# Kernel tuning notes

Measured on AMD Instinct MI355X. Metric: run time of the kernel, lower is better.

Reference implementation:

```python
import jax, jax.numpy as jnp
import numpy as np

TEMPERATURE = 8.0  # sqrt(d_head=64)


def setup_inputs() -> dict:
    key = jax.random.key(0)
    ks = jax.random.split(key, 6)
    shape = (4, 16, 2048, 64)  # [B, H, L, d_head]
    names = ["q_real", "q_imag", "k_real", "k_imag", "v_real", "v_imag"]
    return {n: jax.random.normal(k, shape, dtype=jnp.float32) for n, k in zip(names, ks)}


def reference(q_real, q_imag, k_real, k_imag, v_real, v_imag):
    # attn = | (q / T) @ conj(k)^H |
    # complex matmul with b = conj(k)^T: br = k_r^T, bi = -k_i^T
    qr = q_real / TEMPERATURE
    qi = q_imag / TEMPERATURE
    # [B,H,Lq,Lk]
    s_real = jnp.einsum("bhqd,bhkd->bhqk", qr, k_real) + jnp.einsum("bhqd,bhkd->bhqk", qi, k_imag)
    s_imag = jnp.einsum("bhqd,bhkd->bhqk", qi, k_real) - jnp.einsum("bhqd,bhkd->bhqk", qr, k_imag)
    attn = jax.nn.softmax(jnp.sqrt(s_real * s_real + s_imag * s_imag), axis=-1)
    # dropout p=0.0 (eval) -> identity
    out_real = jnp.einsum("bhqk,bhkd->bhqd", attn, v_real)
    out_imag = jnp.einsum("bhqk,bhkd->bhqd", attn, v_imag)
    # torch.view_as_complex(stack([real, imag], -1)) -> represent as stacked last dim
    output = jnp.stack([out_real, out_imag], axis=-1)  # [B,H,L,d,2]
    return output, attn
```

## Files before the change

kernel.cpp:

```cpp
#include <hip/hip_runtime.h>
#include <hip/hip_bf16.h>

constexpr int kL  = 2048;
constexpr int kD  = 64;
constexpr int kBH = 64;
constexpr size_t kAttnOff = (size_t)kBH * kL * kD * 2;

typedef __bf16 bf16x8 __attribute__((ext_vector_type(8)));
typedef __bf16 bf16x4 __attribute__((ext_vector_type(4)));
typedef float  f32x4  __attribute__((ext_vector_type(4)));
typedef unsigned int u32x4 __attribute__((ext_vector_type(4)));

static __device__ inline bf16x8 neg8(bf16x8 v) {
  u32x4 t = __builtin_bit_cast(u32x4, v);
  t ^= 0x80008000u;
  return __builtin_bit_cast(bf16x8, t);
}

__global__ __launch_bounds__(256) void transpose_v_kernel(
    const float* __restrict__ vr_g, const float* __restrict__ vi_g,
    __hip_bfloat16* __restrict__ vt_r, __hip_bfloat16* __restrict__ vt_i)
{
  __shared__ __align__(16) char lds_raw[2 * 8192];
  char* tr = lds_raw;
  char* ti = lds_raw + 8192;

  const int tid = threadIdx.x;
  const int bh  = blockIdx.x >> 5;
  const int kb  = blockIdx.x & 31;
  const int k0  = kb * 64;

  {
    const int krow = tid >> 2;
    const int d0   = (tid & 3) << 4;
    const size_t gb = ((size_t)bh * kL + k0 + krow) * kD + d0;
    const int base = krow * 128;
    const int swz  = (krow & 7) << 4;
    {
      float4 x0 = *(const float4*)(vr_g + gb);
      float4 x1 = *(const float4*)(vr_g + gb + 4);
      float4 x2 = *(const float4*)(vr_g + gb + 8);
      float4 x3 = *(const float4*)(vr_g + gb + 12);
      bf16x8 p0, p1;
      p0[0]=(__bf16)x0.x; p0[1]=(__bf16)x0.y; p0[2]=(__bf16)x0.z; p0[3]=(__bf16)x0.w;
      p0[4]=(__bf16)x1.x; p0[5]=(__bf16)x1.y; p0[6]=(__bf16)x1.z; p0[7]=(__bf16)x1.w;
      p1[0]=(__bf16)x2.x; p1[1]=(__bf16)x2.y; p1[2]=(__bf16)x2.z; p1[3]=(__bf16)x2.w;
      p1[4]=(__bf16)x3.x; p1[5]=(__bf16)x3.y; p1[6]=(__bf16)x3.z; p1[7]=(__bf16)x3.w;
      *(bf16x8*)(tr + base + ((d0 * 2) ^ swz))      = p0;
      *(bf16x8*)(tr + base + ((d0 * 2 + 16) ^ swz)) = p1;
    }
    {
      float4 x0 = *(const float4*)(vi_g + gb);
      float4 x1 = *(const float4*)(vi_g + gb + 4);
      float4 x2 = *(const float4*)(vi_g + gb + 8);
      float4 x3 = *(const float4*)(vi_g + gb + 12);
      bf16x8 p0, p1;
      p0[0]=(__bf16)x0.x; p0[1]=(__bf16)x0.y; p0[2]=(__bf16)x0.z; p0[3]=(__bf16)x0.w;
      p0[4]=(__bf16)x1.x; p0[5]=(__bf16)x1.y; p0[6]=(__bf16)x1.z; p0[7]=(__bf16)x1.w;
      p1[0]=(__bf16)x2.x; p1[1]=(__bf16)x2.y; p1[2]=(__bf16)x2.z; p1[3]=(__bf16)x2.w;
      p1[4]=(__bf16)x3.x; p1[5]=(__bf16)x3.y; p1[6]=(__bf16)x3.z; p1[7]=(__bf16)x3.w;
      *(bf16x8*)(ti + base + ((d0 * 2) ^ swz))      = p0;
      *(bf16x8*)(ti + base + ((d0 * 2 + 16) ^ swz)) = p1;
    }
  }
  __syncthreads();

  {
    const int d  = tid >> 2;
    const int kc = (tid & 3) << 4;
    const size_t tb = ((size_t)bh * 32 + kb) * 8192;
    char* outr = (char*)vt_r + tb + d * 128;
    char* outi = (char*)vt_i + tb + d * 128;
    const int oswz = (d & 7) << 4;
    bf16x8 pr0, pr1, pi0, pi1;
#pragma unroll
    for (int j = 0; j < 8; ++j) {
      const int k1 = kc + j;
      const int k2 = kc + 8 + j;
      const int b1 = k1 * 128 + ((d * 2) ^ ((k1 & 7) << 4));
      const int b2 = k2 * 128 + ((d * 2) ^ ((k2 & 7) << 4));
      pr0[j] = *(const __bf16*)(tr + b1);
      pr1[j] = *(const __bf16*)(tr + b2);
      pi0[j] = *(const __bf16*)(ti + b1);
      pi1[j] = *(const __bf16*)(ti + b2);
    }
    *(bf16x8*)(outr + ((kc * 2) ^ oswz))        = pr0;
    *(bf16x8*)(outr + ((kc * 2 + 16) ^ oswz))   = pr1;
    *(bf16x8*)(outi + ((kc * 2) ^ oswz))        = pi0;
    *(bf16x8*)(outi + ((kc * 2 + 16) ^ oswz))   = pi1;
  }
}

template<int WS>
__global__ __launch_bounds__(256) void qk_exp_kernel(
    const float* __restrict__ qr_g, const float* __restrict__ qi_g,
    const float* __restrict__ kr_g, const float* __restrict__ ki_g,
    __hip_bfloat16* __restrict__ ews, float* __restrict__ attn,
    float* __restrict__ rowsum)
{
  __shared__ __align__(16) char lds_raw[16384 + 4 * 4096];
  char* kr_l = lds_raw;
  char* ki_l = lds_raw + 8192;
  char* e_l  = lds_raw + 16384 + (threadIdx.x >> 6) * 4096;

  const int tid  = threadIdx.x;
  const int wave = tid >> 6;
  const int lane = tid & 63;
  const int g    = lane >> 4;
  const int r    = lane & 15;

  const int bid = blockIdx.x;
  const int nid = (bid & 7) * 128 + (bid >> 3);
  const int bh  = nid >> 4;
  const int q0w = (nid & 15) * 128 + wave * 32;

  bf16x8 aqr[2][2], aqi[2][2];
#pragma unroll
  for (int qt = 0; qt < 2; ++qt) {
    const size_t qbase = ((size_t)bh * kL + q0w + qt * 16 + r) * kD + g * 8;
#pragma unroll
    for (int f = 0; f < 2; ++f) {
      float4 x0 = *(const float4*)(qr_g + qbase + f * 32);
      float4 x1 = *(const float4*)(qr_g + qbase + f * 32 + 4);
      float4 y0 = *(const float4*)(qi_g + qbase + f * 32);
      float4 y1 = *(const float4*)(qi_g + qbase + f * 32 + 4);
      float xr[8] = {x0.x, x0.y, x0.z, x0.w, x1.x, x1.y, x1.z, x1.w};
      float xi[8] = {y0.x, y0.y, y0.z, y0.w, y1.x, y1.y, y1.z, y1.w};
#pragma unroll
      for (int i = 0; i < 8; ++i) {
        aqr[qt][f][i] = (__bf16)(xr[i] * 0.125f);
        aqi[qt][f][i] = (__bf16)(xi[i] * 0.125f);
      }
    }
  }

  float rs[2] = {0.f, 0.f};

  for (int k0 = 0; k0 < kL; k0 += 64) {
    __syncthreads();
    {
      const int row = tid >> 2;
      const int d0  = (tid & 3) << 4;
      const size_t gb = ((size_t)bh * kL + k0 + row) * kD + d0;
      const int base = row * 128;
      const int swz  = (row & 7) << 4;
      {
        float4 x0 = *(const float4*)(kr_g + gb);
        float4 x1 = *(const float4*)(kr_g + gb + 4);
        float4 x2 = *(const float4*)(kr_g + gb + 8);
        float4 x3 = *(const float4*)(kr_g + gb + 12);
        bf16x8 p0, p1;
        p0[0]=(__bf16)x0.x; p0[1]=(__bf16)x0.y; p0[2]=(__bf16)x0.z; p0[3]=(__bf16)x0.w;
        p0[4]=(__bf16)x1.x; p0[5]=(__bf16)x1.y; p0[6]=(__bf16)x1.z; p0[7]=(__bf16)x1.w;
        p1[0]=(__bf16)x2.x; p1[1]=(__bf16)x2.y; p1[2]=(__bf16)x2.z; p1[3]=(__bf16)x2.w;
        p1[4]=(__bf16)x3.x; p1[5]=(__bf16)x3.y; p1[6]=(__bf16)x3.z; p1[7]=(__bf16)x3.w;
        *(bf16x8*)(kr_l + base + ((d0 * 2) ^ swz))      = p0;
        *(bf16x8*)(kr_l + base + ((d0 * 2 + 16) ^ swz)) = p1;
      }
      {
        float4 x0 = *(const float4*)(ki_g + gb);
        float4 x1 = *(const float4*)(ki_g + gb + 4);
        float4 x2 = *(const float4*)(ki_g + gb + 8);
        float4 x3 = *(const float4*)(ki_g + gb + 12);
        bf16x8 p0, p1;
        p0[0]=(__bf16)x0.x; p0[1]=(__bf16)x0.y; p0[2]=(__bf16)x0.z; p0[3]=(__bf16)x0.w;
        p0[4]=(__bf16)x1.x; p0[5]=(__bf16)x1.y; p0[6]=(__bf16)x1.z; p0[7]=(__bf16)x1.w;
        p1[0]=(__bf16)x2.x; p1[1]=(__bf16)x2.y; p1[2]=(__bf16)x2.z; p1[3]=(__bf16)x2.w;
        p1[4]=(__bf16)x3.x; p1[5]=(__bf16)x3.y; p1[6]=(__bf16)x3.z; p1[7]=(__bf16)x3.w;
        *(bf16x8*)(ki_l + base + ((d0 * 2) ^ swz))      = p0;
        *(bf16x8*)(ki_l + base + ((d0 * 2 + 16) ^ swz)) = p1;
      }
    }
    __syncthreads();

#pragma unroll
    for (int s = 0; s < 4; ++s) {
      const int krow = s * 16 + r;
      const int swz  = (krow & 7) << 4;
      bf16x8 bkr[2], bki[2], bkin[2];
#pragma unroll
      for (int f = 0; f < 2; ++f) {
        const int byte = krow * 128 + (((f * 32 + g * 8) * 2) ^ swz);
        bkr[f]  = *(const bf16x8*)(kr_l + byte);
        bki[f]  = *(const bf16x8*)(ki_l + byte);
        bkin[f] = neg8(bki[f]);
      }
#pragma unroll
      for (int qt = 0; qt < 2; ++qt) {
        f32x4 accr = {0.f, 0.f, 0.f, 0.f};
        f32x4 acci = {0.f, 0.f, 0.f, 0.f};
#pragma unroll
        for (int f = 0; f < 2; ++f) {
          accr = __builtin_amdgcn_mfma_f32_16x16x32_bf16(bkr[f],  aqr[qt][f], accr, 0, 0, 0);
          accr = __builtin_amdgcn_mfma_f32_16x16x32_bf16(bki[f],  aqi[qt][f], accr, 0, 0, 0);
          acci = __builtin_amdgcn_mfma_f32_16x16x32_bf16(bkr[f],  aqi[qt][f], acci, 0, 0, 0);
          acci = __builtin_amdgcn_mfma_f32_16x16x32_bf16(bkin[f], aqr[qt][f], acci, 0, 0, 0);
        }
        float e[4];
#pragma unroll
        for (int i = 0; i < 4; ++i)
          e[i] = __expf(sqrtf(accr[i] * accr[i] + acci[i] * acci[i]));
        rs[qt] += (e[0] + e[1]) + (e[2] + e[3]);
        bf16x4 pe;
#pragma unroll
        for (int i = 0; i < 4; ++i) pe[i] = (__bf16)e[i];
        const int row = qt * 16 + r;
        *(bf16x4*)(e_l + row * 128 + (((s * 16 + g * 4) * 2) ^ ((row & 7) << 4))) = pe;
      }
    }

#pragma unroll
    for (int m = 0; m < 4; ++m) {
      const int row  = m * 8 + (lane >> 3);
      const int byte = row * 128 + (((lane & 7) * 16) ^ ((row & 7) << 4));
      bf16x8 v = *(const bf16x8*)(e_l + byte);
      const size_t base = ((size_t)bh * kL + q0w + row) * kL + k0 + (lane & 7) * 8;
      if (WS) {
        *(bf16x8*)((__bf16*)ews + base) = v;
      } else {
        float4 w0, w1;
        w0.x=(float)v[0]; w0.y=(float)v[1]; w0.z=(float)v[2]; w0.w=(float)v[3];
        w1.x=(float)v[4]; w1.y=(float)v[5]; w1.z=(float)v[6]; w1.w=(float)v[7];
        *(float4*)(attn + base)     = w0;
        *(float4*)(attn + base + 4) = w1;
      }
    }
  }

#pragma unroll
  for (int qt = 0; qt < 2; ++qt) {
    rs[qt] += __shfl_xor(rs[qt], 16, 64);
    rs[qt] += __shfl_xor(rs[qt], 32, 64);
  }
  if (lane < 16) {
#pragma unroll
    for (int qt = 0; qt < 2; ++qt)
      rowsum[(size_t)bh * kL + q0w + qt * 16 + lane] = rs[qt];
  }
}

template<int WS, int VT>
__global__ __launch_bounds__(256) void pv_kernel(
    const float* __restrict__ vr_g, const float* __restrict__ vi_g,
    const __hip_bfloat16* __restrict__ vt_r, const __hip_bfloat16* __restrict__ vt_i,
    const __hip_bfloat16* __restrict__ ews, float* __restrict__ attn,
    const float* __restrict__ rowsum, float* __restrict__ out)
{
  __shared__ __align__(16) char lds_raw[2 * 8192];
  char* vr_l = lds_raw;
  char* vi_l = lds_raw + 8192;

  const int tid  = threadIdx.x;
  const int wave = tid >> 6;
  const int lane = tid & 63;
  const int g    = lane >> 4;
  const int r    = lane & 15;

  const int bid = blockIdx.x;
  const int nid = (bid & 7) * 128 + (bid >> 3);
  const int bh  = nid >> 4;
  const int q0w = (nid & 15) * 128 + wave * 32;

  float invA[2];
#pragma unroll
  for (int qt = 0; qt < 2; ++qt)
    invA[qt] = 1.0f / rowsum[(size_t)bh * kL + q0w + qt * 16 + r];

  f32x4 o_r[2][4], o_i[2][4];
#pragma unroll
  for (int qt = 0; qt < 2; ++qt)
#pragma unroll
    for (int dt = 0; dt < 4; ++dt) {
      o_r[qt][dt] = (f32x4){0.f, 0.f, 0.f, 0.f};
      o_i[qt][dt] = (f32x4){0.f, 0.f, 0.f, 0.f};
    }

  for (int k0 = 0; k0 < kL; k0 += 64) {
    __syncthreads();
    if (VT) {
      const size_t tb = ((size_t)bh * 32 + (k0 >> 6)) * 8192;
      const int o1 = wave * 1024 + lane * 16;
      const int o2 = o1 + 4096;
      *(u32x4*)(vr_l + o1) = *(const u32x4*)((const char*)vt_r + tb + o1);
      *(u32x4*)(vr_l + o2) = *(const u32x4*)((const char*)vt_r + tb + o2);
      *(u32x4*)(vi_l + o1) = *(const u32x4*)((const char*)vt_i + tb + o1);
      *(u32x4*)(vi_l + o2) = *(const u32x4*)((const char*)vt_i + tb + o2);
    } else {
      const int p  = tid >> 3;
      const int d0 = (tid & 7) << 3;
      const size_t gb0 = ((size_t)bh * kL + k0 + 2 * p) * kD + d0;
      const size_t gb1 = gb0 + kD;
      float4 a0 = *(const float4*)(vr_g + gb0);
      float4 a1 = *(const float4*)(vr_g + gb0 + 4);
      float4 a2 = *(const float4*)(vr_g + gb1);
      float4 a3 = *(const float4*)(vr_g + gb1 + 4);
      float4 b0 = *(const float4*)(vi_g + gb0);
      float4 b1 = *(const float4*)(vi_g + gb0 + 4);
      float4 b2 = *(const float4*)(vi_g + gb1);
      float4 b3 = *(const float4*)(vi_g + gb1 + 4);
      float vr0[8] = {a0.x, a0.y, a0.z, a0.w, a1.x, a1.y, a1.z, a1.w};
      float vr1[8] = {a2.x, a2.y, a2.z, a2.w, a3.x, a3.y, a3.z, a3.w};
      float vi0[8] = {b0.x, b0.y, b0.z, b0.w, b1.x, b1.y, b1.z, b1.w};
      float vi1[8] = {b2.x, b2.y, b2.z, b2.w, b3.x, b3.y, b3.z, b3.w};
#pragma unroll
      for (int j = 0; j < 8; ++j) {
        const int d = d0 + j;
        const int byte = d * 128 + ((p * 4) ^ ((d & 7) << 4));
        __bf16 pa[2] = {(__bf16)vr0[j], (__bf16)vr1[j]};
        __bf16 pb[2] = {(__bf16)vi0[j], (__bf16)vi1[j]};
        *(unsigned int*)(vr_l + byte) = *(unsigned int*)pa;
        *(unsigned int*)(vi_l + byte) = *(unsigned int*)pb;
      }
    }
    __syncthreads();

#pragma unroll
    for (int kh = 0; kh < 2; ++kh) {
      bf16x8 af[2];
#pragma unroll
      for (int qt = 0; qt < 2; ++qt) {
        const size_t q = q0w + qt * 16 + r;
        const size_t eb = ((size_t)bh * kL + q) * kL + k0 + kh * 32 + g * 8;
        if (WS) {
          af[qt] = *(const bf16x8*)((const __bf16*)ews + eb);
          float4 w0, w1;
          w0.x = (float)af[qt][0] * invA[qt]; w0.y = (float)af[qt][1] * invA[qt];
          w0.z = (float)af[qt][2] * invA[qt]; w0.w = (float)af[qt][3] * invA[qt];
          w1.x = (float)af[qt][4] * invA[qt]; w1.y = (float)af[qt][5] * invA[qt];
          w1.z = (float)af[qt][6] * invA[qt]; w1.w = (float)af[qt][7] * invA[qt];
          *(float4*)(attn + eb)     = w0;
          *(float4*)(attn + eb + 4) = w1;
        } else {
          float4 e0 = *(const float4*)(attn + eb);
          float4 e1 = *(const float4*)(attn + eb + 4);
          af[qt][0]=(__bf16)e0.x; af[qt][1]=(__bf16)e0.y; af[qt][2]=(__bf16)e0.z; af[qt][3]=(__bf16)e0.w;
          af[qt][4]=(__bf16)e1.x; af[qt][5]=(__bf16)e1.y; af[qt][6]=(__bf16)e1.z; af[qt][7]=(__bf16)e1.w;
          float4 w0 = {e0.x * invA[qt], e0.y * invA[qt], e0.z * invA[qt], e0.w * invA[qt]};
          float4 w1 = {e1.x * invA[qt], e1.y * invA[qt], e1.z * invA[qt], e1.w * invA[qt]};
          *(float4*)(attn + eb)     = w0;
          *(float4*)(attn + eb + 4) = w1;
        }
      }
#pragma unroll
      for (int dt = 0; dt < 4; ++dt) {
        const int d = dt * 16 + r;
        const int byte = d * 128 + (((kh * 32 + g * 8) * 2) ^ ((d & 7) << 4));
        bf16x8 bvr = *(const bf16x8*)(vr_l + byte);
        bf16x8 bvi = *(const bf16x8*)(vi_l + byte);
#pragma unroll
        for (int qt = 0; qt < 2; ++qt) {
          o_r[qt][dt] = __builtin_amdgcn_mfma_f32_16x16x32_bf16(af[qt], bvr, o_r[qt][dt], 0, 0, 0);
          o_i[qt][dt] = __builtin_amdgcn_mfma_f32_16x16x32_bf16(af[qt], bvi, o_i[qt][dt], 0, 0, 0);
        }
      }
    }
  }

#pragma unroll
  for (int qt = 0; qt < 2; ++qt)
#pragma unroll
    for (int i = 0; i < 4; ++i) {
      const size_t q = q0w + qt * 16 + g * 4 + i;
      const float iv = 1.0f / rowsum[(size_t)bh * kL + q];
#pragma unroll
      for (int dt = 0; dt < 4; ++dt) {
        const int d = dt * 16 + r;
        float2 val;
        val.x = o_r[qt][dt][i] * iv;
        val.y = o_i[qt][dt][i] * iv;
        *(float2*)(out + (((size_t)bh * kL + q) * kD + d) * 2) = val;
      }
    }
}

extern "C" void kernel_launch(void* const* d_in, const int* in_sizes, int n_in,
                              void* d_out, int out_size, void* d_ws, size_t ws_size,
                              hipStream_t stream) {
  const float* qr = (const float*)d_in[0];
  const float* qi = (const float*)d_in[1];
  const float* kr = (const float*)d_in[2];
  const float* ki = (const float*)d_in[3];
  const float* vr = (const float*)d_in[4];
  const float* vi = (const float*)d_in[5];
  float* out  = (float*)d_out;
  float* attn = out + kAttnOff;

  float* rowsum = (float*)d_ws;
  const size_t rowsum_bytes = (size_t)kBH * kL * 4;
  __hip_bfloat16* ews = (__hip_bfloat16*)((char*)d_ws + rowsum_bytes);
  const size_t e_bytes = (size_t)kBH * kL * kL * 2;
  const size_t vt_bytes = (size_t)kBH * kD * kL * 2;
  __hip_bfloat16* vt_r = (__hip_bfloat16*)((char*)d_ws + rowsum_bytes + e_bytes);
  __hip_bfloat16* vt_i = vt_r + (size_t)kBH * kD * kL;

  const bool use_ws = (ws_size >= rowsum_bytes + e_bytes);
  const bool use_vt = (ws_size >= rowsum_bytes + e_bytes + 2 * vt_bytes);

  dim3 gridT(kBH * (kL / 64));
  dim3 gridAB(kBH * (kL / 128));

  if (use_vt) {
    transpose_v_kernel<<<gridT, 256, 0, stream>>>(vr, vi, vt_r, vt_i);
    qk_exp_kernel<1><<<gridAB, 256, 0, stream>>>(qr, qi, kr, ki, ews, attn, rowsum);
    pv_kernel<1, 1><<<gridAB, 256, 0, stream>>>(vr, vi, vt_r, vt_i, ews, attn, rowsum, out);
  } else if (use_ws) {
    qk_exp_kernel<1><<<gridAB, 256, 0, stream>>>(qr, qi, kr, ki, ews, attn, rowsum);
    pv_kernel<1, 0><<<gridAB, 256, 0, stream>>>(vr, vi, vt_r, vt_i, ews, attn, rowsum, out);
  } else {
    qk_exp_kernel<0><<<gridAB, 256, 0, stream>>>(qr, qi, kr, ki, ews, attn, rowsum);
    pv_kernel<0, 0><<<gridAB, 256, 0, stream>>>(vr, vi, vt_r, vt_i, ews, attn, rowsum, out);
  }
}
```

Before: 745.8 us.

## Double-buffer K and V tiles in LDS with register prefetch in QK and PV kernels

```diff
diff --git a/kernel.cpp b/kernel.cpp
--- a/kernel.cpp
+++ b/kernel.cpp
@@ -15,6 +15,13 @@
   u32x4 t = __builtin_bit_cast(u32x4, v);
   t ^= 0x80008000u;
   return __builtin_bit_cast(bf16x8, t);
+}
+
+static __device__ inline bf16x8 pack8(const float4& a, const float4& b) {
+  bf16x8 p;
+  p[0]=(__bf16)a.x; p[1]=(__bf16)a.y; p[2]=(__bf16)a.z; p[3]=(__bf16)a.w;
+  p[4]=(__bf16)b.x; p[5]=(__bf16)b.y; p[6]=(__bf16)b.z; p[7]=(__bf16)b.w;
+  return p;
 }
 
 __global__ __launch_bounds__(256) void transpose_v_kernel(
@@ -41,26 +48,16 @@
       float4 x1 = *(const float4*)(vr_g + gb + 4);
       float4 x2 = *(const float4*)(vr_g + gb + 8);
       float4 x3 = *(const float4*)(vr_g + gb + 12);
-      bf16x8 p0, p1;
-      p0[0]=(__bf16)x0.x; p0[1]=(__bf16)x0.y; p0[2]=(__bf16)x0.z; p0[3]=(__bf16)x0.w;
-      p0[4]=(__bf16)x1.x; p0[5]=(__bf16)x1.y; p0[6]=(__bf16)x1.z; p0[7]=(__bf16)x1.w;
-      p1[0]=(__bf16)x2.x; p1[1]=(__bf16)x2.y; p1[2]=(__bf16)x2.z; p1[3]=(__bf16)x2.w;
-      p1[4]=(__bf16)x3.x; p1[5]=(__bf16)x3.y; p1[6]=(__bf16)x3.z; p1[7]=(__bf16)x3.w;
-      *(bf16x8*)(tr + base + ((d0 * 2) ^ swz))      = p0;
-      *(bf16x8*)(tr + base + ((d0 * 2 + 16) ^ swz)) = p1;
+      *(bf16x8*)(tr + base + ((d0 * 2) ^ swz))      = pack8(x0, x1);
+      *(bf16x8*)(tr + base + ((d0 * 2 + 16) ^ swz)) = pack8(x2, x3);
     }
     {
       float4 x0 = *(const float4*)(vi_g + gb);
       float4 x1 = *(const float4*)(vi_g + gb + 4);
       float4 x2 = *(const float4*)(vi_g + gb + 8);
       float4 x3 = *(const float4*)(vi_g + gb + 12);
-      bf16x8 p0, p1;
-      p0[0]=(__bf16)x0.x; p0[1]=(__bf16)x0.y; p0[2]=(__bf16)x0.z; p0[3]=(__bf16)x0.w;
-      p0[4]=(__bf16)x1.x; p0[5]=(__bf16)x1.y; p0[6]=(__bf16)x1.z; p0[7]=(__bf16)x1.w;
-      p1[0]=(__bf16)x2.x; p1[1]=(__bf16)x2.y; p1[2]=(__bf16)x2.z; p1[3]=(__bf16)x2.w;
-      p1[4]=(__bf16)x3.x; p1[5]=(__bf16)x3.y; p1[6]=(__bf16)x3.z; p1[7]=(__bf16)x3.w;
-      *(bf16x8*)(ti + base + ((d0 * 2) ^ swz))      = p0;
-      *(bf16x8*)(ti + base + ((d0 * 2 + 16) ^ swz)) = p1;
+      *(bf16x8*)(ti + base + ((d0 * 2) ^ swz))      = pack8(x0, x1);
+      *(bf16x8*)(ti + base + ((d0 * 2 + 16) ^ swz)) = pack8(x2, x3);
     }
   }
   __syncthreads();
@@ -84,10 +81,10 @@
       pi0[j] = *(const __bf16*)(ti + b1);
       pi1[j] = *(const __bf16*)(ti + b2);
     }
-    *(bf16x8*)(outr + ((kc * 2) ^ oswz))        = pr0;
-    *(bf16x8*)(outr + ((kc * 2 + 16) ^ oswz))   = pr1;
-    *(bf16x8*)(outi + ((kc * 2) ^ oswz))        = pi0;
-    *(bf16x8*)(outi + ((kc * 2 + 16) ^ oswz))   = pi1;
+    *(bf16x8*)(outr + ((kc * 2) ^ oswz))      = pr0;
+    *(bf16x8*)(outr + ((kc * 2 + 16) ^ oswz)) = pr1;
+    *(bf16x8*)(outi + ((kc * 2) ^ oswz))      = pi0;
+    *(bf16x8*)(outi + ((kc * 2 + 16) ^ oswz)) = pi1;
   }
 }
 
@@ -98,10 +95,8 @@
     __hip_bfloat16* __restrict__ ews, float* __restrict__ attn,
     float* __restrict__ rowsum)
 {
-  __shared__ __align__(16) char lds_raw[16384 + 4 * 4096];
-  char* kr_l = lds_raw;
-  char* ki_l = lds_raw + 8192;
-  char* e_l  = lds_raw + 16384 + (threadIdx.x >> 6) * 4096;
+  __shared__ __align__(16) char lds_raw[2 * 16384 + 4 * 4096];
+  char* e_l = lds_raw + 32768 + (threadIdx.x >> 6) * 4096;
 
   const int tid  = threadIdx.x;
   const int wave = tid >> 6;
@@ -114,7 +109,7 @@
   const int bh  = nid >> 4;
   const int q0w = (nid & 15) * 128 + wave * 32;
 
-  bf16x8 aqr[2][2], aqi[2][2];
+  bf16x8 aqr[2][2], aqi[2][2], aqrn[2][2];
 #pragma unroll
   for (int qt = 0; qt < 2; ++qt) {
     const size_t qbase = ((size_t)bh * kL + q0w + qt * 16 + r) * kD + g * 8;
@@ -131,59 +126,47 @@
         aqr[qt][f][i] = (__bf16)(xr[i] * 0.125f);
         aqi[qt][f][i] = (__bf16)(xi[i] * 0.125f);
       }
+      aqrn[qt][f] = neg8(aqr[qt][f]);
     }
   }
 
   float rs[2] = {0.f, 0.f};
 
-  for (int k0 = 0; k0 < kL; k0 += 64) {
-    __syncthreads();
-    {
-      const int row = tid >> 2;
-      const int d0  = (tid & 3) << 4;
-      const size_t gb = ((size_t)bh * kL + k0 + row) * kD + d0;
-      const int base = row * 128;
-      const int swz  = (row & 7) << 4;
-      {
-        float4 x0 = *(const float4*)(kr_g + gb);
-        float4 x1 = *(const float4*)(kr_g + gb + 4);
-        float4 x2 = *(const float4*)(kr_g + gb + 8);
-        float4 x3 = *(const float4*)(kr_g + gb + 12);
-        bf16x8 p0, p1;
-        p0[0]=(__bf16)x0.x; p0[1]=(__bf16)x0.y; p0[2]=(__bf16)x0.z; p0[3]=(__bf16)x0.w;
-        p0[4]=(__bf16)x1.x; p0[5]=(__bf16)x1.y; p0[6]=(__bf16)x1.z; p0[7]=(__bf16)x1.w;
-        p1[0]=(__bf16)x2.x; p1[1]=(__bf16)x2.y; p1[2]=(__bf16)x2.z; p1[3]=(__bf16)x2.w;
-        p1[4]=(__bf16)x3.x; p1[5]=(__bf16)x3.y; p1[6]=(__bf16)x3.z; p1[7]=(__bf16)x3.w;
-        *(bf16x8*)(kr_l + base + ((d0 * 2) ^ swz))      = p0;
-        *(bf16x8*)(kr_l + base + ((d0 * 2 + 16) ^ swz)) = p1;
-      }
-      {
-        float4 x0 = *(const float4*)(ki_g + gb);
-        float4 x1 = *(const float4*)(ki_g + gb + 4);
-        float4 x2 = *(const float4*)(ki_g + gb + 8);
-        float4 x3 = *(const float4*)(ki_g + gb + 12);
-        bf16x8 p0, p1;
-        p0[0]=(__bf16)x0.x; p0[1]=(__bf16)x0.y; p0[2]=(__bf16)x0.z; p0[3]=(__bf16)x0.w;
-        p0[4]=(__bf16)x1.x; p0[5]=(__bf16)x1.y; p0[6]=(__bf16)x1.z; p0[7]=(__bf16)x1.w;
-        p1[0]=(__bf16)x2.x; p1[1]=(__bf16)x2.y; p1[2]=(__bf16)x2.z; p1[3]=(__bf16)x2.w;
-        p1[4]=(__bf16)x3.x; p1[5]=(__bf16)x3.y; p1[6]=(__bf16)x3.z; p1[7]=(__bf16)x3.w;
-        *(bf16x8*)(ki_l + base + ((d0 * 2) ^ swz))      = p0;
-        *(bf16x8*)(ki_l + base + ((d0 * 2 + 16) ^ swz)) = p1;
-      }
-    }
-    __syncthreads();
-
+  const int srow = tid >> 2;
+  const int sd0  = (tid & 3) << 4;
+  float4 kx0, kx1, kx2, kx3, ky0, ky1, ky2, ky3;
+
+  auto LOADK = [&](int t) {
+    const size_t gb = ((size_t)bh * kL + t * 64 + srow) * kD + sd0;
+    kx0 = *(const float4*)(kr_g + gb);
+    kx1 = *(const float4*)(kr_g + gb + 4);
+    kx2 = *(const float4*)(kr_g + gb + 8);
+    kx3 = *(const float4*)(kr_g + gb + 12);
+    ky0 = *(const float4*)(ki_g + gb);
+    ky1 = *(const float4*)(ki_g + gb + 4);
+    ky2 = *(const float4*)(ki_g + gb + 8);
+    ky3 = *(const float4*)(ki_g + gb + 12);
+  };
+  auto WRITEK = [&](char* buf) {
+    const int base = srow * 128;
+    const int swz  = (srow & 7) << 4;
+    *(bf16x8*)(buf + base + ((sd0 * 2) ^ swz))             = pack8(kx0, kx1);
+    *(bf16x8*)(buf + base + ((sd0 * 2 + 16) ^ swz))        = pack8(kx2, kx3);
+    *(bf16x8*)(buf + 8192 + base + ((sd0 * 2) ^ swz))      = pack8(ky0, ky1);
+    *(bf16x8*)(buf + 8192 + base + ((sd0 * 2 + 16) ^ swz)) = pack8(ky2, ky3);
+  };
+
+  auto COMPUTE = [&](const char* kr_l, const char* ki_l, int k0) {
 #pragma unroll
     for (int s = 0; s < 4; ++s) {
       const int krow = s * 16 + r;
       const int swz  = (krow & 7) << 4;
-      bf16x8 bkr[2], bki[2], bkin[2];
+      bf16x8 bkr[2], bki[2];
 #pragma unroll
       for (int f = 0; f < 2; ++f) {
         const int byte = krow * 128 + (((f * 32 + g * 8) * 2) ^ swz);
-        bkr[f]  = *(const bf16x8*)(kr_l + byte);
-        bki[f]  = *(const bf16x8*)(ki_l + byte);
-        bkin[f] = neg8(bki[f]);
+        bkr[f] = *(const bf16x8*)(kr_l + byte);
+        bki[f] = *(const bf16x8*)(ki_l + byte);
       }
 #pragma unroll
       for (int qt = 0; qt < 2; ++qt) {
@@ -191,10 +174,10 @@
         f32x4 acci = {0.f, 0.f, 0.f, 0.f};
 #pragma unroll
         for (int f = 0; f < 2; ++f) {
-          accr = __builtin_amdgcn_mfma_f32_16x16x32_bf16(bkr[f],  aqr[qt][f], accr, 0, 0, 0);
-          accr = __builtin_amdgcn_mfma_f32_16x16x32_bf16(bki[f],  aqi[qt][f], accr, 0, 0, 0);
-          acci = __builtin_amdgcn_mfma_f32_16x16x32_bf16(bkr[f],  aqi[qt][f], acci, 0, 0, 0);
-          acci = __builtin_amdgcn_mfma_f32_16x16x32_bf16(bkin[f], aqr[qt][f], acci, 0, 0, 0);
+          accr = __builtin_amdgcn_mfma_f32_16x16x32_bf16(bkr[f], aqr[qt][f],  accr, 0, 0, 0);
+          accr = __builtin_amdgcn_mfma_f32_16x16x32_bf16(bki[f], aqi[qt][f],  accr, 0, 0, 0);
+          acci = __builtin_amdgcn_mfma_f32_16x16x32_bf16(bkr[f], aqi[qt][f],  acci, 0, 0, 0);
+          acci = __builtin_amdgcn_mfma_f32_16x16x32_bf16(bki[f], aqrn[qt][f], acci, 0, 0, 0);
         }
         float e[4];
 #pragma unroll
@@ -208,7 +191,6 @@
         *(bf16x4*)(e_l + row * 128 + (((s * 16 + g * 4) * 2) ^ ((row & 7) << 4))) = pe;
       }
     }
-
 #pragma unroll
     for (int m = 0; m < 4; ++m) {
       const int row  = m * 8 + (lane >> 3);
@@ -225,6 +207,20 @@
         *(float4*)(attn + base + 4) = w1;
       }
     }
+  };
+
+  LOADK(0);
+  WRITEK(lds_raw);
+  __syncthreads();
+  for (int t = 0; t < 32; ++t) {
+    char* cbuf = lds_raw + (t & 1) * 16384;
+    char* nbuf = lds_raw + ((t + 1) & 1) * 16384;
+    if (t < 31) LOADK(t + 1);
+    COMPUTE(cbuf, cbuf + 8192, t * 64);
+    if (t < 31) {
+      WRITEK(nbuf);
+      __syncthreads();
+    }
   }
 
 #pragma unroll
@@ -239,10 +235,146 @@
   }
 }
 
-template<int WS, int VT>
-__global__ __launch_bounds__(256) void pv_kernel(
+__global__ __launch_bounds__(256) void pv_kernel_db(
+    const __hip_bfloat16* __restrict__ vt_r, const __hip_bfloat16* __restrict__ vt_i,
+    const __hip_bfloat16* __restrict__ ews, float* __restrict__ attn,
+    const float* __restrict__ rowsum, float* __restrict__ out)
+{
+  __shared__ __align__(16) char lds_raw[2 * 16384];
+
+  const int tid  = threadIdx.x;
+  const int wave = tid >> 6;
+  const int lane = tid & 63;
+  const int g    = lane >> 4;
+  const int r    = lane & 15;
+
+  const int bid = blockIdx.x;
+  const int nid = (bid & 7) * 128 + (bid >> 3);
+  const int bh  = nid >> 4;
+  const int q0w = (nid & 15) * 128 + wave * 32;
+
+  float invA[2];
+  size_t ebase[2];
+#pragma unroll
+  for (int qt = 0; qt < 2; ++qt) {
+    invA[qt]  = 1.0f / rowsum[(size_t)bh * kL + q0w + qt * 16 + r];
+    ebase[qt] = ((size_t)bh * kL + q0w + qt * 16 + r) * kL;
+  }
+
+  f32x4 o_r[2][4], o_i[2][4];
+#pragma unroll
+  for (int qt = 0; qt < 2; ++qt)
+#pragma unroll
+    for (int dt = 0; dt < 4; ++dt) {
+      o_r[qt][dt] = (f32x4){0.f, 0.f, 0.f, 0.f};
+      o_i[qt][dt] = (f32x4){0.f, 0.f, 0.f, 0.f};
+    }
+
+  const int o1 = wave * 1024 + lane * 16;
+  const int o2 = o1 + 4096;
+  u32x4 va1, va2, vb1, vb2;
+  const size_t tbase = (size_t)bh * 32 * 8192;
+
+  auto LOADV = [&](int t) {
+    const char* pr = (const char*)vt_r + tbase + (size_t)t * 8192;
+    const char* pi = (const char*)vt_i + tbase + (size_t)t * 8192;
+    va1 = *(const u32x4*)(pr + o1);
+    va2 = *(const u32x4*)(pr + o2);
+    vb1 = *(const u32x4*)(pi + o1);
+    vb2 = *(const u32x4*)(pi + o2);
+  };
+  auto WRITEV = [&](char* buf) {
+    *(u32x4*)(buf + o1)        = va1;
+    *(u32x4*)(buf + o2)        = va2;
+    *(u32x4*)(buf + 8192 + o1) = vb1;
+    *(u32x4*)(buf + 8192 + o2) = vb2;
+  };
+
+  bf16x8 eA[2][2], eB[2][2];
+  auto LOADE = [&](int t, bf16x8 (&er)[2][2]) {
+#pragma unroll
+    for (int kh = 0; kh < 2; ++kh)
+#pragma unroll
+      for (int qt = 0; qt < 2; ++qt)
+        er[kh][qt] = *(const bf16x8*)((const __bf16*)ews + ebase[qt] + t * 64 + kh * 32 + g * 8);
+  };
+
+  auto COMPUTE = [&](const char* vbuf, int t, bf16x8 (&er)[2][2]) {
+    const int k0 = t * 64;
+#pragma unroll
+    for (int kh = 0; kh < 2; ++kh)
+#pragma unroll
+      for (int qt = 0; qt < 2; ++qt) {
+        const size_t eb = ebase[qt] + k0 + kh * 32 + g * 8;
+        float4 w0, w1;
+        w0.x = (float)er[kh][qt][0] * invA[qt]; w0.y = (float)er[kh][qt][1] * invA[qt];
+        w0.z = (float)er[kh][qt][2] * invA[qt]; w0.w = (float)er[kh][qt][3] * invA[qt];
+        w1.x = (float)er[kh][qt][4] * invA[qt]; w1.y = (float)er[kh][qt][5] * invA[qt];
+        w1.z = (float)er[kh][qt][6] * invA[qt]; w1.w = (float)er[kh][qt][7] * invA[qt];
+        *(float4*)(attn + eb)     = w0;
+        *(float4*)(attn + eb + 4) = w1;
+      }
+#pragma unroll
+    for (int kh = 0; kh < 2; ++kh)
+#pragma unroll
+      for (int dt = 0; dt < 4; ++dt) {
+        const int d = dt * 16 + r;
+        const int byte = d * 128 + (((kh * 32 + g * 8) * 2) ^ ((d & 7) << 4));
+        bf16x8 bvr = *(const bf16x8*)(vbuf + byte);
+        bf16x8 bvi = *(const bf16x8*)(vbuf + 8192 + byte);
+#pragma unroll
+        for (int qt = 0; qt < 2; ++qt) {
+          o_r[qt][dt] = __builtin_amdgcn_mfma_f32_16x16x32_bf16(er[kh][qt], bvr, o_r[qt][dt], 0, 0, 0);
+          o_i[qt][dt] = __builtin_amdgcn_mfma_f32_16x16x32_bf16(er[kh][qt], bvi, o_i[qt][dt], 0, 0, 0);
+        }
+      }
+  };
+
+  char* buf0 = lds_raw;
+  char* buf1 = lds_raw + 16384;
+
+  LOADV(0);
+  WRITEV(buf0);
+  LOADE(0, eA);
+  __syncthreads();
+
+  for (int t = 0; t < 32; t += 2) {
+    LOADV(t + 1);
+    LOADE(t + 1, eB);
+    COMPUTE(buf0, t, eA);
+    WRITEV(buf1);
+    __syncthreads();
+    if (t + 2 < 32) {
+      LOADV(t + 2);
+      LOADE(t + 2, eA);
+    }
+    COMPUTE(buf1, t + 1, eB);
+    if (t + 2 < 32) {
+      WRITEV(buf0);
+      __syncthreads();
+    }
+  }
+
+#pragma unroll
+  for (int qt = 0; qt < 2; ++qt)
+#pragma unroll
+    for (int i = 0; i < 4; ++i) {
+      const size_t q = q0w + qt * 16 + g * 4 + i;
+      const float iv = 1.0f / rowsum[(size_t)bh * kL + q];
+#pragma unroll
+      for (int dt = 0; dt < 4; ++dt) {
+        const int d = dt * 16 + r;
+        float2 val;
+        val.x = o_r[qt][dt][i] * iv;
+        val.y = o_i[qt][dt][i] * iv;
+        *(float2*)(out + (((size_t)bh * kL + q) * kD + d) * 2) = val;
+      }
+    }
+}
+
+template<int WS>
+__global__ __launch_bounds__(256) void pv_kernel_legacy(
     const float* __restrict__ vr_g, const float* __restrict__ vi_g,
-    const __hip_bfloat16* __restrict__ vt_r, const __hip_bfloat16* __restrict__ vt_i,
     const __hip_bfloat16* __restrict__ ews, float* __restrict__ attn,
     const float* __restrict__ rowsum, float* __restrict__ out)
 {
@@ -277,15 +409,7 @@
 
   for (int k0 = 0; k0 < kL; k0 += 64) {
     __syncthreads();
-    if (VT) {
-      const size_t tb = ((size_t)bh * 32 + (k0 >> 6)) * 8192;
-      const int o1 = wave * 1024 + lane * 16;
-      const int o2 = o1 + 4096;
-      *(u32x4*)(vr_l + o1) = *(const u32x4*)((const char*)vt_r + tb + o1);
-      *(u32x4*)(vr_l + o2) = *(const u32x4*)((const char*)vt_r + tb + o2);
-      *(u32x4*)(vi_l + o1) = *(const u32x4*)((const char*)vt_i + tb + o1);
-      *(u32x4*)(vi_l + o2) = *(const u32x4*)((const char*)vt_i + tb + o2);
-    } else {
+    {
       const int p  = tid >> 3;
       const int d0 = (tid & 7) << 3;
       const size_t gb0 = ((size_t)bh * kL + k0 + 2 * p) * kD + d0;
@@ -402,12 +526,12 @@
   if (use_vt) {
     transpose_v_kernel<<<gridT, 256, 0, stream>>>(vr, vi, vt_r, vt_i);
     qk_exp_kernel<1><<<gridAB, 256, 0, stream>>>(qr, qi, kr, ki, ews, attn, rowsum);
-    pv_kernel<1, 1><<<gridAB, 256, 0, stream>>>(vr, vi, vt_r, vt_i, ews, attn, rowsum, out);
+    pv_kernel_db<<<gridAB, 256, 0, stream>>>(vt_r, vt_i, ews, attn, rowsum, out);
   } else if (use_ws) {
     qk_exp_kernel<1><<<gridAB, 256, 0, stream>>>(qr, qi, kr, ki, ews, attn, rowsum);
-    pv_kernel<1, 0><<<gridAB, 256, 0, stream>>>(vr, vi, vt_r, vt_i, ews, attn, rowsum, out);
+    pv_kernel_legacy<1><<<gridAB, 256, 0, stream>>>(vr, vi, ews, attn, rowsum, out);
   } else {
     qk_exp_kernel<0><<<gridAB, 256, 0, stream>>>(qr, qi, kr, ki, ews, attn, rowsum);
-    pv_kernel<0, 0><<<gridAB, 256, 0, stream>>>(vr, vi, vt_r, vt_i, ews, attn, rowsum, out);
-  }
-}
+    pv_kernel_legacy<0><<<gridAB, 256, 0, stream>>>(vr, vi, ews, attn, rowsum, out);
+  }
+}
```

New measurement: 755.0 us. No clear change (+1.2%).

## Precast K to bf16 and read K/V fragments directly from global, skipping LDS

Applied to the files above, without the earlier changes.

```diff
diff --git a/kernel.cpp b/kernel.cpp
--- a/kernel.cpp
+++ b/kernel.cpp
@@ -17,9 +17,18 @@
   return __builtin_bit_cast(bf16x8, t);
 }
 
-__global__ __launch_bounds__(256) void transpose_v_kernel(
+static __device__ inline bf16x8 pack8(const float4& a, const float4& b) {
+  bf16x8 p;
+  p[0]=(__bf16)a.x; p[1]=(__bf16)a.y; p[2]=(__bf16)a.z; p[3]=(__bf16)a.w;
+  p[4]=(__bf16)b.x; p[5]=(__bf16)b.y; p[6]=(__bf16)b.z; p[7]=(__bf16)b.w;
+  return p;
+}
+
+__global__ __launch_bounds__(256) void prep_kernel(
+    const float* __restrict__ kr_g, const float* __restrict__ ki_g,
     const float* __restrict__ vr_g, const float* __restrict__ vi_g,
-    __hip_bfloat16* __restrict__ vt_r, __hip_bfloat16* __restrict__ vt_i)
+    __hip_bfloat16* __restrict__ kb_r, __hip_bfloat16* __restrict__ kb_i,
+    __hip_bfloat16* __restrict__ vtp_r, __hip_bfloat16* __restrict__ vtp_i)
 {
   __shared__ __align__(16) char lds_raw[2 * 8192];
   char* tr = lds_raw;
@@ -30,48 +39,45 @@
   const int kb  = blockIdx.x & 31;
   const int k0  = kb * 64;
 
+  const int row = tid >> 2;
+  const int d0  = (tid & 3) << 4;
+  const size_t gb = ((size_t)bh * kL + k0 + row) * kD + d0;
+
   {
-    const int krow = tid >> 2;
-    const int d0   = (tid & 3) << 4;
-    const size_t gb = ((size_t)bh * kL + k0 + krow) * kD + d0;
-    const int base = krow * 128;
-    const int swz  = (krow & 7) << 4;
-    {
-      float4 x0 = *(const float4*)(vr_g + gb);
-      float4 x1 = *(const float4*)(vr_g + gb + 4);
-      float4 x2 = *(const float4*)(vr_g + gb + 8);
-      float4 x3 = *(const float4*)(vr_g + gb + 12);
-      bf16x8 p0, p1;
-      p0[0]=(__bf16)x0.x; p0[1]=(__bf16)x0.y; p0[2]=(__bf16)x0.z; p0[3]=(__bf16)x0.w;
-      p0[4]=(__bf16)x1.x; p0[5]=(__bf16)x1.y; p0[6]=(__bf16)x1.z; p0[7]=(__bf16)x1.w;
-      p1[0]=(__bf16)x2.x; p1[1]=(__bf16)x2.y; p1[2]=(__bf16)x2.z; p1[3]=(__bf16)x2.w;
-      p1[4]=(__bf16)x3.x; p1[5]=(__bf16)x3.y; p1[6]=(__bf16)x3.z; p1[7]=(__bf16)x3.w;
-      *(bf16x8*)(tr + base + ((d0 * 2) ^ swz))      = p0;
-      *(bf16x8*)(tr + base + ((d0 * 2 + 16) ^ swz)) = p1;
-    }
-    {
-      float4 x0 = *(const float4*)(vi_g + gb);
-      float4 x1 = *(const float4*)(vi_g + gb + 4);
-      float4 x2 = *(const float4*)(vi_g + gb + 8);
-      float4 x3 = *(const float4*)(vi_g + gb + 12);
-      bf16x8 p0, p1;
-      p0[0]=(__bf16)x0.x; p0[1]=(__bf16)x0.y; p0[2]=(__bf16)x0.z; p0[3]=(__bf16)x0.w;
-      p0[4]=(__bf16)x1.x; p0[5]=(__bf16)x1.y; p0[6]=(__bf16)x1.z; p0[7]=(__bf16)x1.w;
-      p1[0]=(__bf16)x2.x; p1[1]=(__bf16)x2.y; p1[2]=(__bf16)x2.z; p1[3]=(__bf16)x2.w;
-      p1[4]=(__bf16)x3.x; p1[5]=(__bf16)x3.y; p1[6]=(__bf16)x3.z; p1[7]=(__bf16)x3.w;
-      *(bf16x8*)(ti + base + ((d0 * 2) ^ swz))      = p0;
-      *(bf16x8*)(ti + base + ((d0 * 2 + 16) ^ swz)) = p1;
-    }
+    float4 x0 = *(const float4*)(kr_g + gb);
+    float4 x1 = *(const float4*)(kr_g + gb + 4);
+    float4 x2 = *(const float4*)(kr_g + gb + 8);
+    float4 x3 = *(const float4*)(kr_g + gb + 12);
+    *(bf16x8*)((__bf16*)kb_r + gb)     = pack8(x0, x1);
+    *(bf16x8*)((__bf16*)kb_r + gb + 8) = pack8(x2, x3);
+    float4 y0 = *(const float4*)(ki_g + gb);
+    float4 y1 = *(const float4*)(ki_g + gb + 4);
+    float4 y2 = *(const float4*)(ki_g + gb + 8);
+    float4 y3 = *(const float4*)(ki_g + gb + 12);
+    *(bf16x8*)((__bf16*)kb_i + gb)     = pack8(y0, y1);
+    *(bf16x8*)((__bf16*)kb_i + gb + 8) = pack8(y2, y3);
+  }
+
+  {
+    const int base = row * 128;
+    const int swz  = (row & 7) << 4;
+    float4 x0 = *(const float4*)(vr_g + gb);
+    float4 x1 = *(const float4*)(vr_g + gb + 4);
+    float4 x2 = *(const float4*)(vr_g + gb + 8);
+    float4 x3 = *(const float4*)(vr_g + gb + 12);
+    *(bf16x8*)(tr + base + ((d0 * 2) ^ swz))      = pack8(x0, x1);
+    *(bf16x8*)(tr + base + ((d0 * 2 + 16) ^ swz)) = pack8(x2, x3);
+    float4 y0 = *(const float4*)(vi_g + gb);
+    float4 y1 = *(const float4*)(vi_g + gb + 4);
+    float4 y2 = *(const float4*)(vi_g + gb + 8);
+    float4 y3 = *(const float4*)(vi_g + gb + 12);
+    *(bf16x8*)(ti + base + ((d0 * 2) ^ swz))      = pack8(y0, y1);
+    *(bf16x8*)(ti + base + ((d0 * 2 + 16) ^ swz)) = pack8(y2, y3);
   }
   __syncthreads();
-
   {
     const int d  = tid >> 2;
     const int kc = (tid & 3) << 4;
-    const size_t tb = ((size_t)bh * 32 + kb) * 8192;
-    char* outr = (char*)vt_r + tb + d * 128;
-    char* outi = (char*)vt_i + tb + d * 128;
-    const int oswz = (d & 7) << 4;
     bf16x8 pr0, pr1, pi0, pi1;
 #pragma unroll
     for (int j = 0; j < 8; ++j) {
@@ -84,15 +90,201 @@
       pi0[j] = *(const __bf16*)(ti + b1);
       pi1[j] = *(const __bf16*)(ti + b2);
     }
-    *(bf16x8*)(outr + ((kc * 2) ^ oswz))        = pr0;
-    *(bf16x8*)(outr + ((kc * 2 + 16) ^ oswz))   = pr1;
-    *(bf16x8*)(outi + ((kc * 2) ^ oswz))        = pi0;
-    *(bf16x8*)(outi + ((kc * 2 + 16) ^ oswz))   = pi1;
-  }
+    const size_t ob = ((size_t)bh * kD + d) * kL + k0 + kc;
+    *(bf16x8*)((__bf16*)vtp_r + ob)     = pr0;
+    *(bf16x8*)((__bf16*)vtp_r + ob + 8) = pr1;
+    *(bf16x8*)((__bf16*)vtp_i + ob)     = pi0;
+    *(bf16x8*)((__bf16*)vtp_i + ob + 8) = pi1;
+  }
+}
+
+__global__ __launch_bounds__(256) void qk_direct(
+    const float* __restrict__ qr_g, const float* __restrict__ qi_g,
+    const __hip_bfloat16* __restrict__ kb_r, const __hip_bfloat16* __restrict__ kb_i,
+    __hip_bfloat16* __restrict__ ews, float* __restrict__ rowsum)
+{
+  __shared__ __align__(16) char e_lds[4 * 4096];
+  char* e_l = e_lds + (threadIdx.x >> 6) * 4096;
+
+  const int tid  = threadIdx.x;
+  const int wave = tid >> 6;
+  const int lane = tid & 63;
+  const int g    = lane >> 4;
+  const int r    = lane & 15;
+
+  const int bid = blockIdx.x;
+  const int nid = (bid & 7) * 128 + (bid >> 3);
+  const int bh  = nid >> 4;
+  const int q0w = (nid & 15) * 128 + wave * 32;
+
+  bf16x8 aqr[2][2], aqi[2][2];
+#pragma unroll
+  for (int qt = 0; qt < 2; ++qt) {
+    const size_t qbase = ((size_t)bh * kL + q0w + qt * 16 + r) * kD + g * 8;
+#pragma unroll
+    for (int f = 0; f < 2; ++f) {
+      float4 x0 = *(const float4*)(qr_g + qbase + f * 32);
+      float4 x1 = *(const float4*)(qr_g + qbase + f * 32 + 4);
+      float4 y0 = *(const float4*)(qi_g + qbase + f * 32);
+      float4 y1 = *(const float4*)(qi_g + qbase + f * 32 + 4);
+      float xr[8] = {x0.x, x0.y, x0.z, x0.w, x1.x, x1.y, x1.z, x1.w};
+      float xi[8] = {y0.x, y0.y, y0.z, y0.w, y1.x, y1.y, y1.z, y1.w};
+#pragma unroll
+      for (int i = 0; i < 8; ++i) {
+        aqr[qt][f][i] = (__bf16)(xr[i] * 0.125f);
+        aqi[qt][f][i] = (__bf16)(xi[i] * 0.125f);
+      }
+    }
+  }
+
+  float rs[2] = {0.f, 0.f};
+
+#pragma unroll 1
+  for (int t = 0; t < 32; ++t) {
+    const int k0 = t * 64;
+#pragma unroll
+    for (int s = 0; s < 4; ++s) {
+      const size_t krow = (size_t)bh * kL + k0 + s * 16 + r;
+      const __bf16* kr_p = (const __bf16*)kb_r + krow * kD + g * 8;
+      const __bf16* ki_p = (const __bf16*)kb_i + krow * kD + g * 8;
+      bf16x8 bkr[2], bki[2], bkin[2];
+#pragma unroll
+      for (int f = 0; f < 2; ++f) {
+        bkr[f]  = *(const bf16x8*)(kr_p + f * 32);
+        bki[f]  = *(const bf16x8*)(ki_p + f * 32);
+        bkin[f] = neg8(bki[f]);
+      }
+#pragma unroll
+      for (int qt = 0; qt < 2; ++qt) {
+        f32x4 accr = {0.f, 0.f, 0.f, 0.f};
+        f32x4 acci = {0.f, 0.f, 0.f, 0.f};
+#pragma unroll
+        for (int f = 0; f < 2; ++f) {
+          accr = __builtin_amdgcn_mfma_f32_16x16x32_bf16(bkr[f],  aqr[qt][f], accr, 0, 0, 0);
+          accr = __builtin_amdgcn_mfma_f32_16x16x32_bf16(bki[f],  aqi[qt][f], accr, 0, 0, 0);
+          acci = __builtin_amdgcn_mfma_f32_16x16x32_bf16(bkr[f],  aqi[qt][f], acci, 0, 0, 0);
+          acci = __builtin_amdgcn_mfma_f32_16x16x32_bf16(bkin[f], aqr[qt][f], acci, 0, 0, 0);
+        }
+        float e[4];
+#pragma unroll
+        for (int i = 0; i < 4; ++i)
+          e[i] = __expf(sqrtf(accr[i] * accr[i] + acci[i] * acci[i]));
+        rs[qt] += (e[0] + e[1]) + (e[2] + e[3]);
+        bf16x4 pe;
+#pragma unroll
+        for (int i = 0; i < 4; ++i) pe[i] = (__bf16)e[i];
+        const int row = qt * 16 + r;
+        *(bf16x4*)(e_l + row * 128 + (((s * 16 + g * 4) * 2) ^ ((row & 7) << 4))) = pe;
+      }
+    }
+#pragma unroll
+    for (int m = 0; m < 4; ++m) {
+      const int row  = m * 8 + (lane >> 3);
+      const int byte = row * 128 + (((lane & 7) * 16) ^ ((row & 7) << 4));
+      bf16x8 v = *(const bf16x8*)(e_l + byte);
+      const size_t base = ((size_t)bh * kL + q0w + row) * kL + k0 + (lane & 7) * 8;
+      *(bf16x8*)((__bf16*)ews + base) = v;
+    }
+  }
+
+#pragma unroll
+  for (int qt = 0; qt < 2; ++qt) {
+    rs[qt] += __shfl_xor(rs[qt], 16, 64);
+    rs[qt] += __shfl_xor(rs[qt], 32, 64);
+  }
+  if (lane < 16) {
+#pragma unroll
+    for (int qt = 0; qt < 2; ++qt)
+      rowsum[(size_t)bh * kL + q0w + qt * 16 + lane] = rs[qt];
+  }
+}
+
+__global__ __launch_bounds__(256) void pv_direct(
+    const __hip_bfloat16* __restrict__ vtp_r, const __hip_bfloat16* __restrict__ vtp_i,
+    const __hip_bfloat16* __restrict__ ews, float* __restrict__ attn,
+    const float* __restrict__ rowsum, float* __restrict__ out)
+{
+  const int tid  = threadIdx.x;
+  const int wave = tid >> 6;
+  const int lane = tid & 63;
+  const int g    = lane >> 4;
+  const int r    = lane & 15;
+
+  const int bid = blockIdx.x;
+  const int nid = (bid & 7) * 128 + (bid >> 3);
+  const int bh  = nid >> 4;
+  const int q0w = (nid & 15) * 128 + wave * 32;
+
+  float invA[2];
+  size_t ebase[2];
+#pragma unroll
+  for (int qt = 0; qt < 2; ++qt) {
+    invA[qt]  = 1.0f / rowsum[(size_t)bh * kL + q0w + qt * 16 + r];
+    ebase[qt] = ((size_t)bh * kL + q0w + qt * 16 + r) * kL;
+  }
+
+  f32x4 o_r[2][4], o_i[2][4];
+#pragma unroll
+  for (int qt = 0; qt < 2; ++qt)
+#pragma unroll
+    for (int dt = 0; dt < 4; ++dt) {
+      o_r[qt][dt] = (f32x4){0.f, 0.f, 0.f, 0.f};
+      o_i[qt][dt] = (f32x4){0.f, 0.f, 0.f, 0.f};
+    }
+
+#pragma unroll 1
+  for (int t = 0; t < 32; ++t) {
+    const int k0 = t * 64;
+    bf16x8 ef[2][2];
+#pragma unroll
+    for (int kh = 0; kh < 2; ++kh)
+#pragma unroll
+      for (int qt = 0; qt < 2; ++qt) {
+        const size_t eb = ebase[qt] + k0 + kh * 32 + g * 8;
+        bf16x8 v = *(const bf16x8*)((const __bf16*)ews + eb);
+        ef[kh][qt] = v;
+        float4 w0, w1;
+        w0.x = (float)v[0] * invA[qt]; w0.y = (float)v[1] * invA[qt];
+        w0.z = (float)v[2] * invA[qt]; w0.w = (float)v[3] * invA[qt];
+        w1.x = (float)v[4] * invA[qt]; w1.y = (float)v[5] * invA[qt];
+        w1.z = (float)v[6] * invA[qt]; w1.w = (float)v[7] * invA[qt];
+        *(float4*)(attn + eb)     = w0;
+        *(float4*)(attn + eb + 4) = w1;
+      }
+#pragma unroll
+    for (int kh = 0; kh < 2; ++kh)
+#pragma unroll
+      for (int dt = 0; dt < 4; ++dt) {
+        const size_t vb = ((size_t)bh * kD + dt * 16 + r) * kL + k0 + kh * 32 + g * 8;
+        bf16x8 bvr = *(const bf16x8*)((const __bf16*)vtp_r + vb);
+        bf16x8 bvi = *(const bf16x8*)((const __bf16*)vtp_i + vb);
+#pragma unroll
+        for (int qt = 0; qt < 2; ++qt) {
+          o_r[qt][dt] = __builtin_amdgcn_mfma_f32_16x16x32_bf16(ef[kh][qt], bvr, o_r[qt][dt], 0, 0, 0);
+          o_i[qt][dt] = __builtin_amdgcn_mfma_f32_16x16x32_bf16(ef[kh][qt], bvi, o_i[qt][dt], 0, 0, 0);
+        }
+      }
+  }
+
+#pragma unroll
+  for (int qt = 0; qt < 2; ++qt)
+#pragma unroll
+    for (int i = 0; i < 4; ++i) {
+      const size_t q = q0w + qt * 16 + g * 4 + i;
+      const float iv = 1.0f / rowsum[(size_t)bh * kL + q];
+#pragma unroll
+      for (int dt = 0; dt < 4; ++dt) {
+        const int d = dt * 16 + r;
+        float2 val;
+        val.x = o_r[qt][dt][i] * iv;
+        val.y = o_i[qt][dt][i] * iv;
+        *(float2*)(out + (((size_t)bh * kL + q) * kD + d) * 2) = val;
+      }
+    }
 }
 
 template<int WS>
-__global__ __launch_bounds__(256) void qk_exp_kernel(
+__global__ __launch_bounds__(256) void qk_exp_legacy(
     const float* __restrict__ qr_g, const float* __restrict__ qi_g,
     const float* __restrict__ kr_g, const float* __restrict__ ki_g,
     __hip_bfloat16* __restrict__ ews, float* __restrict__ attn,
@@ -149,26 +341,16 @@
         float4 x1 = *(const float4*)(kr_g + gb + 4);
         float4 x2 = *(const float4*)(kr_g + gb + 8);
         float4 x3 = *(const float4*)(kr_g + gb + 12);
-        bf16x8 p0, p1;
-        p0[0]=(__bf16)x0.x; p0[1]=(__bf16)x0.y; p0[2]=(__bf16)x0.z; p0[3]=(__bf16)x0.w;
-        p0[4]=(__bf16)x1.x; p0[5]=(__bf16)x1.y; p0[6]=(__bf16)x1.z; p0[7]=(__bf16)x1.w;
-        p1[0]=(__bf16)x2.x; p1[1]=(__bf16)x2.y; p1[2]=(__bf16)x2.z; p1[3]=(__bf16)x2.w;
-        p1[4]=(__bf16)x3.x; p1[5]=(__bf16)x3.y; p1[6]=(__bf16)x3.z; p1[7]=(__bf16)x3.w;
-        *(bf16x8*)(kr_l + base + ((d0 * 2) ^ swz))      = p0;
-        *(bf16x8*)(kr_l + base + ((d0 * 2 + 16) ^ swz)) = p1;
+        *(bf16x8*)(kr_l + base + ((d0 * 2) ^ swz))      = pack8(x0, x1);
+        *(bf16x8*)(kr_l + base + ((d0 * 2 + 16) ^ swz)) = pack8(x2, x3);
       }
       {
         float4 x0 = *(const float4*)(ki_g + gb);
         float4 x1 = *(const float4*)(ki_g + gb + 4);
         float4 x2 = *(const float4*)(ki_g + gb + 8);
         float4 x3 = *(const float4*)(ki_g + gb + 12);
-        bf16x8 p0, p1;
-        p0[0]=(__bf16)x0.x; p0[1]=(__bf16)x0.y; p0[2]=(__bf16)x0.z; p0[3]=(__bf16)x0.w;
-        p0[4]=(__bf16)x1.x; p0[5]=(__bf16)x1.y; p0[6]=(__bf16)x1.z; p0[7]=(__bf16)x1.w;
-        p1[0]=(__bf16)x2.x; p1[1]=(__bf16)x2.y; p1[2]=(__bf16)x2.z; p1[3]=(__bf16)x2.w;
-        p1[4]=(__bf16)x3.x; p1[5]=(__bf16)x3.y; p1[6]=(__bf16)x3.z; p1[7]=(__bf16)x3.w;
-        *(bf16x8*)(ki_l + base + ((d0 * 2) ^ swz))      = p0;
-        *(bf16x8*)(ki_l + base + ((d0 * 2 + 16) ^ swz)) = p1;
+        *(bf16x8*)(ki_l + base + ((d0 * 2) ^ swz))      = pack8(x0, x1);
+        *(bf16x8*)(ki_l + base + ((d0 * 2 + 16) ^ swz)) = pack8(x2, x3);
       }
     }
     __syncthreads();
@@ -239,10 +421,9 @@
   }
 }
 
-template<int WS, int VT>
-__global__ __launch_bounds__(256) void pv_kernel(
+template<int WS>
+__global__ __launch_bounds__(256) void pv_legacy(
     const float* __restrict__ vr_g, const float* __restrict__ vi_g,
-    const __hip_bfloat16* __restrict__ vt_r, const __hip_bfloat16* __restrict__ vt_i,
     const __hip_bfloat16* __restrict__ ews, float* __restrict__ attn,
     const float* __restrict__ rowsum, float* __restrict__ out)
 {
@@ -277,15 +458,7 @@
 
   for (int k0 = 0; k0 < kL; k0 += 64) {
     __syncthreads();
-    if (VT) {
-      const size_t tb = ((size_t)bh * 32 + (k0 >> 6)) * 8192;
-      const int o1 = wave * 1024 + lane * 16;
-      const int o2 = o1 + 4096;
-      *(u32x4*)(vr_l + o1) = *(const u32x4*)((const char*)vt_r + tb + o1);
-      *(u32x4*)(vr_l + o2) = *(const u32x4*)((const char*)vt_r + tb + o2);
-      *(u32x4*)(vi_l + o1) = *(const u32x4*)((const char*)vt_i + tb + o1);
-      *(u32x4*)(vi_l + o2) = *(const u32x4*)((const char*)vt_i + tb + o2);
-    } else {
+    {
       const int p  = tid >> 3;
       const int d0 = (tid & 7) << 3;
       const size_t gb0 = ((size_t)bh * kL + k0 + 2 * p) * kD + d0;
@@ -389,25 +562,28 @@
   const size_t rowsum_bytes = (size_t)kBH * kL * 4;
   __hip_bfloat16* ews = (__hip_bfloat16*)((char*)d_ws + rowsum_bytes);
   const size_t e_bytes = (size_t)kBH * kL * kL * 2;
-  const size_t vt_bytes = (size_t)kBH * kD * kL * 2;
-  __hip_bfloat16* vt_r = (__hip_bfloat16*)((char*)d_ws + rowsum_bytes + e_bytes);
-  __hip_bfloat16* vt_i = vt_r + (size_t)kBH * kD * kL;
-
-  const bool use_ws = (ws_size >= rowsum_bytes + e_bytes);
-  const bool use_vt = (ws_size >= rowsum_bytes + e_bytes + 2 * vt_bytes);
-
-  dim3 gridT(kBH * (kL / 64));
+  const size_t aux_bytes = (size_t)kBH * kD * kL * 2;
+  char* aux = (char*)d_ws + rowsum_bytes + e_bytes;
+  __hip_bfloat16* vtp_r = (__hip_bfloat16*)aux;
+  __hip_bfloat16* vtp_i = (__hip_bfloat16*)(aux + aux_bytes);
+  __hip_bfloat16* kb_r  = (__hip_bfloat16*)(aux + 2 * aux_bytes);
+  __hip_bfloat16* kb_i  = (__hip_bfloat16*)(aux + 3 * aux_bytes);
+
+  const bool use_ws     = (ws_size >= rowsum_bytes + e_bytes);
+  const bool use_direct = (ws_size >= rowsum_bytes + e_bytes + 4 * aux_bytes);
+
+  dim3 gridP(kBH * (kL / 64));
   dim3 gridAB(kBH * (kL / 128));
 
-  if (use_vt) {
-    transpose_v_kernel<<<gridT, 256, 0, stream>>>(vr, vi, vt_r, vt_i);
-    qk_exp_kernel<1><<<gridAB, 256, 0, stream>>>(qr, qi, kr, ki, ews, attn, rowsum);
-    pv_kernel<1, 1><<<gridAB, 256, 0, stream>>>(vr, vi, vt_r, vt_i, ews, attn, rowsum, out);
+  if (use_direct) {
+    prep_kernel<<<gridP, 256, 0, stream>>>(kr, ki, vr, vi, kb_r, kb_i, vtp_r, vtp_i);
+    qk_direct<<<gridAB, 256, 0, stream>>>(qr, qi, kb_r, kb_i, ews, rowsum);
+    pv_direct<<<gridAB, 256, 0, stream>>>(vtp_r, vtp_i, ews, attn, rowsum, out);
   } else if (use_ws) {
-    qk_exp_kernel<1><<<gridAB, 256, 0, stream>>>(qr, qi, kr, ki, ews, attn, rowsum);
-    pv_kernel<1, 0><<<gridAB, 256, 0, stream>>>(vr, vi, vt_r, vt_i, ews, attn, rowsum, out);
+    qk_exp_legacy<1><<<gridAB, 256, 0, stream>>>(qr, qi, kr, ki, ews, attn, rowsum);
+    pv_legacy<1><<<gridAB, 256, 0, stream>>>(vr, vi, ews, attn, rowsum, out);
   } else {
-    qk_exp_kernel<0><<<gridAB, 256, 0, stream>>>(qr, qi, kr, ki, ews, attn, rowsum);
-    pv_kernel<0, 0><<<gridAB, 256, 0, stream>>>(vr, vi, vt_r, vt_i, ews, attn, rowsum, out);
-  }
-}
+    qk_exp_legacy<0><<<gridAB, 256, 0, stream>>>(qr, qi, kr, ki, ews, attn, rowsum);
+    pv_legacy<0><<<gridAB, 256, 0, stream>>>(vr, vi, ews, attn, rowsum, out);
+  }
+}
```

After: 982.7 us. 31.8% more time.
